# Kernel tuning notes

Hardware: AMD Instinct MI355X
Metric: run time of the kernel (lower is better)

## Reference

```python
import jax, jax.numpy as jnp
import numpy as np

DECAY = 0.9
BETA_OBS = 1.0
BETA_STATE = 1.0

N_OBS = 20000
N_STATES = 1024
N_ACTIONS = 64
STATE_DIM = 256
RFD = 2048


def setup_inputs() -> dict:
    key = jax.random.key(0)
    ks = jax.random.split(key, 7)
    Q = jax.random.normal(ks[0], (STATE_DIM, N_STATES), dtype=jnp.float32) / np.sqrt(STATE_DIM).astype(np.float32)
    V = jax.random.normal(ks[1], (STATE_DIM, N_ACTIONS), dtype=jnp.float32) / np.sqrt(STATE_DIM).astype(np.float32)
    W = jax.random.normal(ks[2], (RFD, STATE_DIM), dtype=jnp.float32)
    M_re = jax.random.normal(ks[3], (RFD, N_OBS), dtype=jnp.float32)
    M_im = jax.random.normal(ks[4], (RFD, N_OBS), dtype=jnp.float32)
    obs = jax.random.uniform(ks[5], (N_OBS,), dtype=jnp.float32)
    action = jax.random.uniform(ks[6], (N_ACTIONS,), dtype=jnp.float32)
    return {"Q": Q, "V": V, "W": W, "M_re": M_re, "M_im": M_im, "obs": obs, "action": action}


def reference(Q, V, W, M_re, M_im, obs, action):
    # One fused POCML step: memory write (decayed outer product), state
    # rotation via complex random-feature phase, clean_up (state-kernel
    # softmax retrieval), and obs retrieval from memory.
    D = W.shape[0]  # random_feature_dim
    M = M_re + 1j * M_im                       # [D, n_obs] complex64
    obs_c = obs.astype(jnp.complex64)
    # get_state_from_memory
    state0 = M @ obs_c                         # [D]
    # update_memory: M *= decay; M += outer(state, obs)
    M_new = DECAY * M + jnp.outer(state0, obs_c)
    # update_state: v = V @ action; phi_v = exp(1j * W @ v); state *= phi_v
    v = V @ action                             # [state_dim]
    phi_v = jnp.exp(1j * (W @ v))              # [D] complex64
    state1 = state0 * phi_v
    # clean_up: phi_Q = exp(1j * W @ Q), weights = softmax(beta*sim(phi_Q.T, state))
    phi_Q = jnp.exp(1j * (W @ Q))              # [D, n_states]
    score = BETA_STATE * (phi_Q.T @ jnp.conj(state1)).real / D  # [n_states]
    weights = jax.nn.softmax(score)
    state2 = phi_Q @ weights.astype(jnp.complex64)              # [D]
    # get_obs_from_memory: softmax(beta_obs * sim(M.T, state))
    obs_score = BETA_OBS * (M_new.T @ jnp.conj(state2)).real / D  # [n_obs]
    return jax.nn.softmax(obs_score)
```

## Files before the change

### kernel.cpp

```cpp
#include <hip/hip_runtime.h>
#include <math.h>

#define N_OBS    20000
#define N_OBS4   5000
#define N_STATES 1024
#define N_ACT    64
#define SDIM     256
#define RFD      2048
#define DECAY    0.9f

typedef float v4f __attribute__((ext_vector_type(4)));

__device__ __forceinline__ v4f ntload4(const float* p) {
    return __builtin_nontemporal_load((const v4f*)p);
}

#define OFF_SCORE  0
#define OFF_OBSACC 1024
#define ZERO_CNT   (OFF_OBSACC + N_OBS)
#define OFF_S0RE   21024
#define OFF_S0IM   23072
#define OFF_S1RE   25120
#define OFF_S1IM   27168
#define OFF_S2RE   29216
#define OFF_S2IM   31264
#define OFF_WTS    33312
#define OFF_COSQ   34816
#define OFF_SINQ   (34816 + RFD*N_STATES)
#define WS_FLOATS  (OFF_SINQ + RFD*N_STATES)
#define OFF_P0RE   OFF_COSQ
#define OFF_P0IM   (OFF_COSQ + 10*RFD)

__global__ __launch_bounds__(256) void k_state0(
    const float* __restrict__ Mre, const float* __restrict__ Mim,
    const float* __restrict__ obs, float* __restrict__ p0re, float* __restrict__ p0im)
{
    const int d = blockIdx.y;
    const int seg = blockIdx.x;
    const int tid = threadIdx.x;
    const float* mr = Mre + (size_t)d * N_OBS + seg * 2000;
    const float* mi = Mim + (size_t)d * N_OBS + seg * 2000;
    const float4* ob = (const float4*)obs + seg * 500;
    float ar = 0.f, ai = 0.f;
    #pragma unroll
    for (int it = 0; it < 2; ++it) {
        int i = tid + it * 256;
        if (i < 500) {
            float4 o = ob[i];
            v4f a = ntload4(mr + i * 4);
            v4f b = ntload4(mi + i * 4);
            ar += a.x*o.x + a.y*o.y + a.z*o.z + a.w*o.w;
            ai += b.x*o.x + b.y*o.y + b.z*o.z + b.w*o.w;
        }
    }
    #pragma unroll
    for (int off = 32; off > 0; off >>= 1) {
        ar += __shfl_down(ar, off);
        ai += __shfl_down(ai, off);
    }
    __shared__ float pr[4], pi[4];
    const int wave = tid >> 6, lane = tid & 63;
    if (lane == 0) { pr[wave] = ar; pi[wave] = ai; }
    __syncthreads();
    if (tid == 0) {
        p0re[seg * RFD + d] = pr[0] + pr[1] + pr[2] + pr[3];
        p0im[seg * RFD + d] = pi[0] + pi[1] + pi[2] + pi[3];
    }
}

__global__ __launch_bounds__(256) void k_state1(
    const float* __restrict__ V, const float* __restrict__ action,
    const float* __restrict__ W,
    const float* __restrict__ p0re, const float* __restrict__ p0im,
    float* __restrict__ s0re, float* __restrict__ s0im,
    float* __restrict__ s1re, float* __restrict__ s1im)
{
    __shared__ float vsh[SDIM];
    const int tid = threadIdx.x;
    float acc = 0.f;
    for (int a = 0; a < N_ACT; a++) acc += V[tid * N_ACT + a] * action[a];
    vsh[tid] = acc;
    __syncthreads();
    const int d = blockIdx.x * 256 + tid;
    float re = 0.f, im = 0.f;
    #pragma unroll
    for (int s = 0; s < 10; s++) {
        re += p0re[s * RFD + d];
        im += p0im[s * RFD + d];
    }
    s0re[d] = re; s0im[d] = im;
    const float* wr = W + (size_t)d * SDIM;
    float th = 0.f;
    #pragma unroll 8
    for (int k = 0; k < SDIM; k++) th += wr[k] * vsh[k];
    float sn, cs;
    sincosf(th, &sn, &cs);
    s1re[d] = re * cs - im * sn;
    s1im[d] = re * sn + im * cs;
}

__global__ __launch_bounds__(256) void k_phiQ(
    const float* __restrict__ W, const float* __restrict__ Q,
    const float* __restrict__ s1re, const float* __restrict__ s1im,
    float* __restrict__ cosQ, float* __restrict__ sinQ, float* __restrict__ score)
{
    __shared__ float As[16][65];
    __shared__ float Bs[16][64];
    __shared__ float sscore[64];
    const int tid = threadIdx.x;
    const int tx = tid & 15;
    const int ty = tid >> 4;
    const int m0 = blockIdx.y * 64;
    const int n0 = blockIdx.x * 64;
    float c[4][4] = {};
    for (int k0 = 0; k0 < SDIM; k0 += 16) {
        {
            int k = tid & 15, mb = tid >> 4;
            #pragma unroll
            for (int j = 0; j < 4; j++)
                As[k][mb + 16*j] = W[(size_t)(m0 + mb + 16*j) * SDIM + k0 + k];
        }
        {
            int n = tid & 63, kb = tid >> 6;
            #pragma unroll
            for (int j = 0; j < 4; j++)
                Bs[kb + 4*j][n] = Q[(size_t)(k0 + kb + 4*j) * N_STATES + n0 + n];
        }
        __syncthreads();
        #pragma unroll
        for (int kk = 0; kk < 16; kk++) {
            float a[4], b[4];
            #pragma unroll
            for (int i = 0; i < 4; i++) a[i] = As[kk][ty*4 + i];
            #pragma unroll
            for (int j = 0; j < 4; j++) b[j] = Bs[kk][tx*4 + j];
            #pragma unroll
            for (int i = 0; i < 4; i++)
                #pragma unroll
                for (int j = 0; j < 4; j++)
                    c[i][j] += a[i] * b[j];
        }
        __syncthreads();
    }
    if (tid < 64) sscore[tid] = 0.f;
    __syncthreads();
    float sre[4], sim[4];
    #pragma unroll
    for (int i = 0; i < 4; i++) {
        int d = m0 + ty*4 + i;
        sre[i] = s1re[d]; sim[i] = s1im[d];
    }
    #pragma unroll
    for (int j = 0; j < 4; j++) {
        float pj = 0.f;
        #pragma unroll
        for (int i = 0; i < 4; i++) {
            int d = m0 + ty*4 + i;
            int s = n0 + tx*4 + j;
            float sn, cs;
            sincosf(c[i][j], &sn, &cs);
            cosQ[(size_t)d * N_STATES + s] = cs;
            sinQ[(size_t)d * N_STATES + s] = sn;
            pj += cs * sre[i] + sn * sim[i];
        }
        atomicAdd(&sscore[tx*4 + j], pj);
    }
    __syncthreads();
    if (tid < 64) atomicAdd(&score[n0 + tid], sscore[tid]);
}

__global__ __launch_bounds__(256) void k_softmax_w(
    const float* __restrict__ score, float* __restrict__ wts)
{
    __shared__ float red[256];
    const int tid = threadIdx.x;
    const float scale = 1.f / (float)RFD;
    float4 v = ((const float4*)score)[tid];
    v.x *= scale; v.y *= scale; v.z *= scale; v.w *= scale;
    float mx = fmaxf(fmaxf(v.x, v.y), fmaxf(v.z, v.w));
    red[tid] = mx; __syncthreads();
    for (int s = 128; s > 0; s >>= 1) {
        if (tid < s) red[tid] = fmaxf(red[tid], red[tid+s]);
        __syncthreads();
    }
    mx = red[0]; __syncthreads();
    float4 e;
    e.x = expf(v.x - mx); e.y = expf(v.y - mx);
    e.z = expf(v.z - mx); e.w = expf(v.w - mx);
    red[tid] = e.x + e.y + e.z + e.w; __syncthreads();
    for (int s = 128; s > 0; s >>= 1) {
        if (tid < s) red[tid] += red[tid+s];
        __syncthreads();
    }
    const float inv = 1.f / red[0];
    e.x *= inv; e.y *= inv; e.z *= inv; e.w *= inv;
    ((float4*)wts)[tid] = e;
}

__global__ __launch_bounds__(256) void k_state2(
    const float* __restrict__ cosQ, const float* __restrict__ sinQ,
    const float* __restrict__ wts,
    float* __restrict__ s2re, float* __restrict__ s2im)
{
    __shared__ float r1[256], r2[256];
    const int d = blockIdx.x, tid = threadIdx.x;
    float4 w = ((const float4*)wts)[tid];
    float4 a = ((const float4*)(cosQ + (size_t)d * N_STATES))[tid];
    float4 b = ((const float4*)(sinQ + (size_t)d * N_STATES))[tid];
    r1[tid] = a.x*w.x + a.y*w.y + a.z*w.z + a.w*w.w;
    r2[tid] = b.x*w.x + b.y*w.y + b.z*w.z + b.w*w.w;
    __syncthreads();
    for (int s = 128; s > 0; s >>= 1) {
        if (tid < s) { r1[tid] += r1[tid+s]; r2[tid] += r2[tid+s]; }
        __syncthreads();
    }
    if (tid == 0) { s2re[d] = r1[0]; s2im[d] = r2[0]; }
}

__global__ __launch_bounds__(256) void k_obs_acc(
    const float* __restrict__ Mre, const float* __restrict__ Mim,
    const float* __restrict__ s2re, const float* __restrict__ s2im,
    float* __restrict__ obs_acc)
{
    __shared__ float c_s[32], s_s[32];
    const int tid = threadIdx.x;
    const int dbase = blockIdx.y * 32;
    if (tid < 32) { c_s[tid] = s2re[dbase + tid]; s_s[tid] = s2im[dbase + tid]; }
    __syncthreads();
    const int idx = blockIdx.x * 256 + tid;
    if (idx < N_OBS4) {
        float4 acc = make_float4(0.f, 0.f, 0.f, 0.f);
        #pragma unroll 8
        for (int j = 0; j < 32; j++) {
            size_t base = ((size_t)(dbase + j) * N_OBS4 + idx) * 4;
            v4f a = ntload4(Mre + base);
            v4f b = ntload4(Mim + base);
            float cc = c_s[j], ss = s_s[j];
            acc.x += a.x*cc + b.x*ss;
            acc.y += a.y*cc + b.y*ss;
            acc.z += a.z*cc + b.z*ss;
            acc.w += a.w*cc + b.w*ss;
        }
        atomicAdd(&obs_acc[idx*4 + 0], acc.x);
        atomicAdd(&obs_acc[idx*4 + 1], acc.y);
        atomicAdd(&obs_acc[idx*4 + 2], acc.z);
        atomicAdd(&obs_acc[idx*4 + 3], acc.w);
    }
}

__global__ __launch_bounds__(1024) void k_softmax_obs(
    const float* __restrict__ obs_acc, const float* __restrict__ obs,
    const float* __restrict__ s0re, const float* __restrict__ s0im,
    const float* __restrict__ s2re, const float* __restrict__ s2im,
    float* __restrict__ out)
{
    __shared__ float red[1024];
    const int tid = threadIdx.x;
    float dp = 0.f;
    #pragma unroll
    for (int i = 0; i < 2; i++) {
        int d = tid + i * 1024;
        dp += s0re[d] * s2re[d] + s0im[d] * s2im[d];
    }
    red[tid] = dp; __syncthreads();
    for (int s = 512; s > 0; s >>= 1) {
        if (tid < s) red[tid] += red[tid+s];
        __syncthreads();
    }
    const float d0 = red[0];
    __syncthreads();
    const float scale = 1.f / (float)RFD;
    float vals[20];
    float mx = -3.402823466e+38f;
    #pragma unroll
    for (int i = 0; i < 20; i++) {
        int idx = tid + i * 1024;
        if (idx < N_OBS) {
            float sc = (DECAY * obs_acc[idx] + obs[idx] * d0) * scale;
            vals[i] = sc;
            mx = fmaxf(mx, sc);
        } else vals[i] = -3.402823466e+38f;
    }
    red[tid] = mx; __syncthreads();
    for (int s = 512; s > 0; s >>= 1) {
        if (tid < s) red[tid] = fmaxf(red[tid], red[tid+s]);
        __syncthreads();
    }
    mx = red[0]; __syncthreads();
    float sum = 0.f;
    #pragma unroll
    for (int i = 0; i < 20; i++) {
        int idx = tid + i * 1024;
        if (idx < N_OBS) {
            vals[i] = expf(vals[i] - mx);
            sum += vals[i];
        }
    }
    red[tid] = sum; __syncthreads();
    for (int s = 512; s > 0; s >>= 1) {
        if (tid < s) red[tid] += red[tid+s];
        __syncthreads();
    }
    const float inv = 1.f / red[0];
    #pragma unroll
    for (int i = 0; i < 20; i++) {
        int idx = tid + i * 1024;
        if (idx < N_OBS) out[idx] = vals[i] * inv;
    }
}

extern "C" void kernel_launch(void* const* d_in, const int* in_sizes, int n_in,
                              void* d_out, int out_size, void* d_ws, size_t ws_size,
                              hipStream_t stream) {
    const float* Q      = (const float*)d_in[0];
    const float* V      = (const float*)d_in[1];
    const float* W      = (const float*)d_in[2];
    const float* Mre    = (const float*)d_in[3];
    const float* Mim    = (const float*)d_in[4];
    const float* obs    = (const float*)d_in[5];
    const float* action = (const float*)d_in[6];
    float* out = (float*)d_out;
    float* ws  = (float*)d_ws;

    if (ws_size < (size_t)WS_FLOATS * sizeof(float)) return;

    float* score = ws + OFF_SCORE;
    float* oacc  = ws + OFF_OBSACC;
    float* s0re  = ws + OFF_S0RE;
    float* s0im  = ws + OFF_S0IM;
    float* s1re  = ws + OFF_S1RE;
    float* s1im  = ws + OFF_S1IM;
    float* s2re  = ws + OFF_S2RE;
    float* s2im  = ws + OFF_S2IM;
    float* wts   = ws + OFF_WTS;
    float* cosQ  = ws + OFF_COSQ;
    float* sinQ  = ws + OFF_SINQ;
    float* p0re  = ws + OFF_P0RE;
    float* p0im  = ws + OFF_P0IM;

    hipMemsetAsync(ws, 0, (size_t)ZERO_CNT * sizeof(float), stream);

    k_state0<<<dim3(10, RFD), 256, 0, stream>>>(Mre, Mim, obs, p0re, p0im);
    k_state1<<<RFD / 256, 256, 0, stream>>>(V, action, W, p0re, p0im, s0re, s0im, s1re, s1im);
    k_phiQ<<<dim3(N_STATES / 64, RFD / 64), 256, 0, stream>>>(W, Q, s1re, s1im, cosQ, sinQ, score);
    k_softmax_w<<<1, 256, 0, stream>>>(score, wts);
    k_state2<<<RFD, 256, 0, stream>>>(cosQ, sinQ, wts, s2re, s2im);
    k_obs_acc<<<dim3((N_OBS4 + 255) / 256, RFD / 32), 256, 0, stream>>>(Mre, Mim, s2re, s2im, oacc);
    k_softmax_obs<<<1, 1024, 0, stream>>>(oacc, obs, s0re, s0im, s2re, s2im, out);
}
```

Measured before the change: 442.7 us.

## Fuse independent phiQ GEMM and state0 reduction into one heterogeneous launch

The phiQ GEMM+sincos, the V@action product and the M@obs reduction are independent, so they now run as different block ranges of a single kernel. This lets the compute-bound GEMM overlap with the bandwidth-bound memory read. The score projection is split out into a separate k_score kernel that rereads cosQ/sinQ. state1 now uses one wave per row with a shuffle reduction. obs_acc is retiled to 16 rows per block with split accumulators, which doubles its atomics, and the extra score pass adds traffic over cosQ/sinQ.

```diff
diff --git a/kernel.cpp b/kernel.cpp
--- a/kernel.cpp
+++ b/kernel.cpp
@@ -25,148 +25,163 @@
 #define OFF_S2RE   29216
 #define OFF_S2IM   31264
 #define OFF_WTS    33312
+#define OFF_VWS    34336
 #define OFF_COSQ   34816
-#define OFF_SINQ   (34816 + RFD*N_STATES)
-#define WS_FLOATS  (OFF_SINQ + RFD*N_STATES)
-#define OFF_P0RE   OFF_COSQ
-#define OFF_P0IM   (OFF_COSQ + 10*RFD)
-
-__global__ __launch_bounds__(256) void k_state0(
+#define OFF_SINQ   (OFF_COSQ + RFD*N_STATES)
+#define OFF_P0RE   (OFF_SINQ + RFD*N_STATES)
+#define OFF_P0IM   (OFF_P0RE + 5*RFD)
+#define WS_FLOATS  (OFF_P0IM + 5*RFD)
+
+#define NB_GEMM   512
+#define NB_STATE0 (5 * RFD)
+#define NB_FUSED  (NB_GEMM + 1 + NB_STATE0)
+
+__global__ __launch_bounds__(256) void k_fused(
     const float* __restrict__ Mre, const float* __restrict__ Mim,
-    const float* __restrict__ obs, float* __restrict__ p0re, float* __restrict__ p0im)
-{
-    const int d = blockIdx.y;
-    const int seg = blockIdx.x;
-    const int tid = threadIdx.x;
-    const float* mr = Mre + (size_t)d * N_OBS + seg * 2000;
-    const float* mi = Mim + (size_t)d * N_OBS + seg * 2000;
-    const float4* ob = (const float4*)obs + seg * 500;
-    float ar = 0.f, ai = 0.f;
-    #pragma unroll
-    for (int it = 0; it < 2; ++it) {
-        int i = tid + it * 256;
-        if (i < 500) {
-            float4 o = ob[i];
-            v4f a = ntload4(mr + i * 4);
-            v4f b = ntload4(mi + i * 4);
-            ar += a.x*o.x + a.y*o.y + a.z*o.z + a.w*o.w;
-            ai += b.x*o.x + b.y*o.y + b.z*o.z + b.w*o.w;
-        }
-    }
-    #pragma unroll
-    for (int off = 32; off > 0; off >>= 1) {
-        ar += __shfl_down(ar, off);
-        ai += __shfl_down(ai, off);
-    }
-    __shared__ float pr[4], pi[4];
-    const int wave = tid >> 6, lane = tid & 63;
-    if (lane == 0) { pr[wave] = ar; pi[wave] = ai; }
-    __syncthreads();
-    if (tid == 0) {
-        p0re[seg * RFD + d] = pr[0] + pr[1] + pr[2] + pr[3];
-        p0im[seg * RFD + d] = pi[0] + pi[1] + pi[2] + pi[3];
+    const float* __restrict__ obs,
+    const float* __restrict__ W, const float* __restrict__ Q,
+    const float* __restrict__ V, const float* __restrict__ action,
+    float* __restrict__ cosQ, float* __restrict__ sinQ,
+    float* __restrict__ p0re, float* __restrict__ p0im,
+    float* __restrict__ vout)
+{
+    const int b = blockIdx.x;
+    const int tid = threadIdx.x;
+
+    if (b < NB_GEMM) {
+        __shared__ float As[16][65];
+        __shared__ float Bs[16][64];
+        const int tx = tid & 15;
+        const int ty = tid >> 4;
+        const int m0 = (b >> 4) * 64;
+        const int n0 = (b & 15) * 64;
+        float c[4][4] = {};
+        for (int k0 = 0; k0 < SDIM; k0 += 16) {
+            {
+                int k = tid & 15, mb = tid >> 4;
+                #pragma unroll
+                for (int j = 0; j < 4; j++)
+                    As[k][mb + 16*j] = W[(size_t)(m0 + mb + 16*j) * SDIM + k0 + k];
+            }
+            {
+                int n = tid & 63, kb = tid >> 6;
+                #pragma unroll
+                for (int j = 0; j < 4; j++)
+                    Bs[kb + 4*j][n] = Q[(size_t)(k0 + kb + 4*j) * N_STATES + n0 + n];
+            }
+            __syncthreads();
+            #pragma unroll
+            for (int kk = 0; kk < 16; kk++) {
+                float a[4], bb[4];
+                #pragma unroll
+                for (int i = 0; i < 4; i++) a[i] = As[kk][ty*4 + i];
+                #pragma unroll
+                for (int j = 0; j < 4; j++) bb[j] = Bs[kk][tx*4 + j];
+                #pragma unroll
+                for (int i = 0; i < 4; i++)
+                    #pragma unroll
+                    for (int j = 0; j < 4; j++)
+                        c[i][j] += a[i] * bb[j];
+            }
+            __syncthreads();
+        }
+        #pragma unroll
+        for (int i = 0; i < 4; i++) {
+            int d = m0 + ty*4 + i;
+            #pragma unroll
+            for (int j = 0; j < 4; j++) {
+                int s = n0 + tx*4 + j;
+                float sn, cs;
+                sincosf(c[i][j], &sn, &cs);
+                cosQ[(size_t)d * N_STATES + s] = cs;
+                sinQ[(size_t)d * N_STATES + s] = sn;
+            }
+        }
+    } else if (b == NB_GEMM) {
+        float acc = 0.f;
+        for (int a = 0; a < N_ACT; a++) acc += V[tid * N_ACT + a] * action[a];
+        vout[tid] = acc;
+    } else {
+        const int bb = b - (NB_GEMM + 1);
+        const int d = bb / 5;
+        const int seg = bb - d * 5;
+        const float* mr = Mre + (size_t)d * N_OBS;
+        const float* mi = Mim + (size_t)d * N_OBS;
+        const float4* ob = (const float4*)obs;
+        float ar[4] = {}, ai[4] = {};
+        #pragma unroll
+        for (int it = 0; it < 4; ++it) {
+            int i = seg * 1024 + it * 256 + tid;
+            bool ok = i < N_OBS4;
+            int ic = ok ? i : 0;
+            float4 o = ok ? ob[ic] : make_float4(0.f, 0.f, 0.f, 0.f);
+            v4f a = ntload4(mr + 4 * (size_t)ic);
+            v4f m = ntload4(mi + 4 * (size_t)ic);
+            ar[it] += a.x*o.x + a.y*o.y + a.z*o.z + a.w*o.w;
+            ai[it] += m.x*o.x + m.y*o.y + m.z*o.z + m.w*o.w;
+        }
+        float arr = (ar[0] + ar[1]) + (ar[2] + ar[3]);
+        float aii = (ai[0] + ai[1]) + (ai[2] + ai[3]);
+        #pragma unroll
+        for (int off = 32; off > 0; off >>= 1) {
+            arr += __shfl_down(arr, off);
+            aii += __shfl_down(aii, off);
+        }
+        __shared__ float pr[4], pi[4];
+        const int wave = tid >> 6, lane = tid & 63;
+        if (lane == 0) { pr[wave] = arr; pi[wave] = aii; }
+        __syncthreads();
+        if (tid == 0) {
+            p0re[seg * RFD + d] = pr[0] + pr[1] + pr[2] + pr[3];
+            p0im[seg * RFD + d] = pi[0] + pi[1] + pi[2] + pi[3];
+        }
     }
 }
 
 __global__ __launch_bounds__(256) void k_state1(
-    const float* __restrict__ V, const float* __restrict__ action,
-    const float* __restrict__ W,
+    const float* __restrict__ W, const float* __restrict__ vws,
     const float* __restrict__ p0re, const float* __restrict__ p0im,
     float* __restrict__ s0re, float* __restrict__ s0im,
     float* __restrict__ s1re, float* __restrict__ s1im)
 {
-    __shared__ float vsh[SDIM];
-    const int tid = threadIdx.x;
+    const int tid = threadIdx.x;
+    const int w = tid >> 6, l = tid & 63;
+    const int d = blockIdx.x * 4 + w;
+    float4 wv = ((const float4*)(W + (size_t)d * SDIM))[l];
+    float4 vv = ((const float4*)vws)[l];
+    float th = wv.x*vv.x + wv.y*vv.y + wv.z*vv.z + wv.w*vv.w;
+    #pragma unroll
+    for (int off = 32; off > 0; off >>= 1) th += __shfl_down(th, off);
+    if (l == 0) {
+        float re = 0.f, im = 0.f;
+        #pragma unroll
+        for (int s = 0; s < 5; s++) {
+            re += p0re[s * RFD + d];
+            im += p0im[s * RFD + d];
+        }
+        s0re[d] = re; s0im[d] = im;
+        float sn, cs;
+        sincosf(th, &sn, &cs);
+        s1re[d] = re * cs - im * sn;
+        s1im[d] = re * sn + im * cs;
+    }
+}
+
+__global__ __launch_bounds__(256) void k_score(
+    const float* __restrict__ cosQ, const float* __restrict__ sinQ,
+    const float* __restrict__ s1re, const float* __restrict__ s1im,
+    float* __restrict__ score)
+{
+    const int s = blockIdx.x * 256 + threadIdx.x;
+    const int d0 = blockIdx.y * 32;
     float acc = 0.f;
-    for (int a = 0; a < N_ACT; a++) acc += V[tid * N_ACT + a] * action[a];
-    vsh[tid] = acc;
-    __syncthreads();
-    const int d = blockIdx.x * 256 + tid;
-    float re = 0.f, im = 0.f;
-    #pragma unroll
-    for (int s = 0; s < 10; s++) {
-        re += p0re[s * RFD + d];
-        im += p0im[s * RFD + d];
-    }
-    s0re[d] = re; s0im[d] = im;
-    const float* wr = W + (size_t)d * SDIM;
-    float th = 0.f;
-    #pragma unroll 8
-    for (int k = 0; k < SDIM; k++) th += wr[k] * vsh[k];
-    float sn, cs;
-    sincosf(th, &sn, &cs);
-    s1re[d] = re * cs - im * sn;
-    s1im[d] = re * sn + im * cs;
-}
-
-__global__ __launch_bounds__(256) void k_phiQ(
-    const float* __restrict__ W, const float* __restrict__ Q,
-    const float* __restrict__ s1re, const float* __restrict__ s1im,
-    float* __restrict__ cosQ, float* __restrict__ sinQ, float* __restrict__ score)
-{
-    __shared__ float As[16][65];
-    __shared__ float Bs[16][64];
-    __shared__ float sscore[64];
-    const int tid = threadIdx.x;
-    const int tx = tid & 15;
-    const int ty = tid >> 4;
-    const int m0 = blockIdx.y * 64;
-    const int n0 = blockIdx.x * 64;
-    float c[4][4] = {};
-    for (int k0 = 0; k0 < SDIM; k0 += 16) {
-        {
-            int k = tid & 15, mb = tid >> 4;
-            #pragma unroll
-            for (int j = 0; j < 4; j++)
-                As[k][mb + 16*j] = W[(size_t)(m0 + mb + 16*j) * SDIM + k0 + k];
-        }
-        {
-            int n = tid & 63, kb = tid >> 6;
-            #pragma unroll
-            for (int j = 0; j < 4; j++)
-                Bs[kb + 4*j][n] = Q[(size_t)(k0 + kb + 4*j) * N_STATES + n0 + n];
-        }
-        __syncthreads();
-        #pragma unroll
-        for (int kk = 0; kk < 16; kk++) {
-            float a[4], b[4];
-            #pragma unroll
-            for (int i = 0; i < 4; i++) a[i] = As[kk][ty*4 + i];
-            #pragma unroll
-            for (int j = 0; j < 4; j++) b[j] = Bs[kk][tx*4 + j];
-            #pragma unroll
-            for (int i = 0; i < 4; i++)
-                #pragma unroll
-                for (int j = 0; j < 4; j++)
-                    c[i][j] += a[i] * b[j];
-        }
-        __syncthreads();
-    }
-    if (tid < 64) sscore[tid] = 0.f;
-    __syncthreads();
-    float sre[4], sim[4];
-    #pragma unroll
-    for (int i = 0; i < 4; i++) {
-        int d = m0 + ty*4 + i;
-        sre[i] = s1re[d]; sim[i] = s1im[d];
-    }
-    #pragma unroll
-    for (int j = 0; j < 4; j++) {
-        float pj = 0.f;
-        #pragma unroll
-        for (int i = 0; i < 4; i++) {
-            int d = m0 + ty*4 + i;
-            int s = n0 + tx*4 + j;
-            float sn, cs;
-            sincosf(c[i][j], &sn, &cs);
-            cosQ[(size_t)d * N_STATES + s] = cs;
-            sinQ[(size_t)d * N_STATES + s] = sn;
-            pj += cs * sre[i] + sn * sim[i];
-        }
-        atomicAdd(&sscore[tx*4 + j], pj);
-    }
-    __syncthreads();
-    if (tid < 64) atomicAdd(&score[n0 + tid], sscore[tid]);
+    #pragma unroll 4
+    for (int j = 0; j < 32; j++) {
+        int d = d0 + j;
+        acc += cosQ[(size_t)d * N_STATES + s] * s1re[d]
+             + sinQ[(size_t)d * N_STATES + s] * s1im[d];
+    }
+    atomicAdd(&score[s], acc);
 }
 
 __global__ __launch_bounds__(256) void k_softmax_w(
@@ -222,29 +237,37 @@
     const float* __restrict__ s2re, const float* __restrict__ s2im,
     float* __restrict__ obs_acc)
 {
-    __shared__ float c_s[32], s_s[32];
-    const int tid = threadIdx.x;
-    const int dbase = blockIdx.y * 32;
-    if (tid < 32) { c_s[tid] = s2re[dbase + tid]; s_s[tid] = s2im[dbase + tid]; }
+    __shared__ float c_s[16], s_s[16];
+    const int tid = threadIdx.x;
+    const int dbase = blockIdx.y * 16;
+    if (tid < 16) { c_s[tid] = s2re[dbase + tid]; s_s[tid] = s2im[dbase + tid]; }
     __syncthreads();
     const int idx = blockIdx.x * 256 + tid;
     if (idx < N_OBS4) {
-        float4 acc = make_float4(0.f, 0.f, 0.f, 0.f);
-        #pragma unroll 8
-        for (int j = 0; j < 32; j++) {
+        float4 acc[4];
+        #pragma unroll
+        for (int u = 0; u < 4; u++) acc[u] = make_float4(0.f, 0.f, 0.f, 0.f);
+        #pragma unroll
+        for (int j = 0; j < 16; j++) {
             size_t base = ((size_t)(dbase + j) * N_OBS4 + idx) * 4;
             v4f a = ntload4(Mre + base);
             v4f b = ntload4(Mim + base);
             float cc = c_s[j], ss = s_s[j];
-            acc.x += a.x*cc + b.x*ss;
-            acc.y += a.y*cc + b.y*ss;
-            acc.z += a.z*cc + b.z*ss;
-            acc.w += a.w*cc + b.w*ss;
-        }
-        atomicAdd(&obs_acc[idx*4 + 0], acc.x);
-        atomicAdd(&obs_acc[idx*4 + 1], acc.y);
-        atomicAdd(&obs_acc[idx*4 + 2], acc.z);
-        atomicAdd(&obs_acc[idx*4 + 3], acc.w);
+            int u = j & 3;
+            acc[u].x += a.x*cc + b.x*ss;
+            acc[u].y += a.y*cc + b.y*ss;
+            acc[u].z += a.z*cc + b.z*ss;
+            acc[u].w += a.w*cc + b.w*ss;
+        }
+        float4 t;
+        t.x = (acc[0].x + acc[1].x) + (acc[2].x + acc[3].x);
+        t.y = (acc[0].y + acc[1].y) + (acc[2].y + acc[3].y);
+        t.z = (acc[0].z + acc[1].z) + (acc[2].z + acc[3].z);
+        t.w = (acc[0].w + acc[1].w) + (acc[2].w + acc[3].w);
+        atomicAdd(&obs_acc[idx*4 + 0], t.x);
+        atomicAdd(&obs_acc[idx*4 + 1], t.y);
+        atomicAdd(&obs_acc[idx*4 + 2], t.z);
+        atomicAdd(&obs_acc[idx*4 + 3], t.w);
     }
 }
 
@@ -333,6 +356,7 @@
     float* s2re  = ws + OFF_S2RE;
     float* s2im  = ws + OFF_S2IM;
     float* wts   = ws + OFF_WTS;
+    float* vws   = ws + OFF_VWS;
     float* cosQ  = ws + OFF_COSQ;
     float* sinQ  = ws + OFF_SINQ;
     float* p0re  = ws + OFF_P0RE;
@@ -340,11 +364,12 @@
 
     hipMemsetAsync(ws, 0, (size_t)ZERO_CNT * sizeof(float), stream);
 
-    k_state0<<<dim3(10, RFD), 256, 0, stream>>>(Mre, Mim, obs, p0re, p0im);
-    k_state1<<<RFD / 256, 256, 0, stream>>>(V, action, W, p0re, p0im, s0re, s0im, s1re, s1im);
-    k_phiQ<<<dim3(N_STATES / 64, RFD / 64), 256, 0, stream>>>(W, Q, s1re, s1im, cosQ, sinQ, score);
+    k_fused<<<NB_FUSED, 256, 0, stream>>>(Mre, Mim, obs, W, Q, V, action,
+                                          cosQ, sinQ, p0re, p0im, vws);
+    k_state1<<<RFD / 4, 256, 0, stream>>>(W, vws, p0re, p0im, s0re, s0im, s1re, s1im);
+    k_score<<<dim3(4, 64), 256, 0, stream>>>(cosQ, sinQ, s1re, s1im, score);
     k_softmax_w<<<1, 256, 0, stream>>>(score, wts);
     k_state2<<<RFD, 256, 0, stream>>>(cosQ, sinQ, wts, s2re, s2im);
-    k_obs_acc<<<dim3((N_OBS4 + 255) / 256, RFD / 32), 256, 0, stream>>>(Mre, Mim, s2re, s2im, oacc);
+    k_obs_acc<<<dim3((N_OBS4 + 255) / 256, RFD / 16), 256, 0, stream>>>(Mre, Mim, s2re, s2im, oacc);
     k_softmax_obs<<<1, 1024, 0, stream>>>(oacc, obs, s0re, s0im, s2re, s2im, out);
 }
```

Result: faster. 421.3 us (-4.8%).
